# Kernel optimization log

Hardware: AMD Instinct MI355X
Metric: run time of the kernel (lower is better)

## Reference

```python
import jax, jax.numpy as jnp
import numpy as np

B, S, H, NH, MAXLEN = 4, 1024, 2048, 16, 1024
HD = H // NH  # head_dim = 128

def setup_inputs() -> dict:
    key = jax.random.key(0)
    ks = jax.random.split(key, 16)
    def lin(i):
        # torch Linear default init ~ U(-1/sqrt(in), 1/sqrt(in)); store W as [in, out]
        bound = 1.0 / np.sqrt(H)
        W = jax.random.uniform(ks[i], (H, H), jnp.float32, -bound, bound)
        b = jax.random.uniform(ks[i + 1], (H,), jnp.float32, -bound, bound)
        return W, b
    Wq, bq = lin(0)
    Wk, bk = lin(2)
    Wv, bv = lin(4)
    Wu, bu = lin(6)
    Wf2, bf2 = lin(8)
    rel_table = jax.random.normal(ks[10], (2 * MAXLEN - 1, NH), jnp.float32)
    query = jax.random.normal(ks[11], (B, S, H), jnp.float32)
    key_t = jax.random.normal(ks[12], (B, S, H), jnp.float32)
    value = jax.random.normal(ks[13], (B, S, H), jnp.float32)
    # causal mask [B, Sq, Sk]
    attn_mask = jnp.broadcast_to(jnp.tril(jnp.ones((S, S), bool)), (B, S, S))
    return {"query": query, "key": key_t, "value": value, "attn_mask": attn_mask,
            "Wq": Wq, "bq": bq, "Wk": Wk, "bk": bk, "Wv": Wv, "bv": bv,
            "Wu": Wu, "bu": bu, "Wf2": Wf2, "bf2": bf2, "rel_table": rel_table}

def reference(query, key, value, attn_mask, Wq, bq, Wk, bk, Wv, bv, Wu, bu, Wf2, bf2, rel_table):
    silu = jax.nn.silu
    U = silu(query @ Wu + bu)                      # [B,S,H]
    Q = silu(query @ Wq + bq).reshape(B, S, NH, HD).transpose(0, 2, 1, 3)  # [B,NH,S,HD]
    K = silu(key @ Wk + bk).reshape(B, S, NH, HD).transpose(0, 2, 1, 3)
    V = silu(value @ Wv + bv).reshape(B, S, NH, HD).transpose(0, 2, 1, 3)
    scale = HD ** -0.5
    scores = jnp.einsum('bhqd,bhkd->bhqk', Q, K) * scale  # [B,NH,S,S]
    # relative position bias lookup (non-infer path)
    positions = jnp.arange(S)[:, None] - jnp.arange(S)[None, :]
    rel_idx = positions + MAXLEN - 1                       # [S,S]
    rel_bias = rel_table[rel_idx].transpose(2, 0, 1)[None]  # [1,NH,S,S]
    scores = scores + rel_bias
    attn = silu(scores)  # SiLU attention instead of softmax
    attn = jnp.where(attn_mask[:, None, :, :], attn, 0.0)
    out = jnp.einsum('bhqk,bhkd->bhqd', attn, V)           # [B,NH,S,HD]
    out = out.transpose(0, 2, 1, 3).reshape(B, S, H)
    gated = out * U
    return gated @ Wf2 + bf2
```

## Files before the change

### kernel.cpp

```cpp
#include <hip/hip_runtime.h>
#include <stdint.h>

#define HDIM 2048
#define SEQLEN 1024
#define NHEADS 16
#define HEADD 128

typedef unsigned short u16;
typedef unsigned int u32;
typedef __attribute__((ext_vector_type(8))) short bf16x8;
typedef __attribute__((ext_vector_type(8))) u16 u16x8;
typedef __attribute__((ext_vector_type(4))) u16 u16x4;
typedef __attribute__((ext_vector_type(4))) float f32x4;

__device__ __forceinline__ float bf2f(u16 u) {
    union { u32 i; float f; } v; v.i = ((u32)u) << 16; return v.f;
}
__device__ __forceinline__ u16 f2bf(float f) {
    union { float f; u32 i; } v; v.f = f;
    return (u16)((v.i + 0x7fffu + ((v.i >> 16) & 1u)) >> 16);
}
__device__ __forceinline__ u16 f2bf_t(float f) {
    union { float f; u32 i; } v; v.f = f; return (u16)(v.i >> 16);
}
__device__ __forceinline__ float silu_f(float x) {
    return x * __builtin_amdgcn_rcpf(1.f + __expf(-x));
}
__device__ __forceinline__ void glds16(const void* g, void* l) {
    __builtin_amdgcn_global_load_lds(
        (const __attribute__((address_space(1))) u32*)g,
        (__attribute__((address_space(3))) u32*)l, 16, 0, 0);
}

__global__ __launch_bounds__(256) void f32_to_bf16(const float* __restrict__ in,
                                                   u16* __restrict__ out, int n8) {
    int i = blockIdx.x * 256 + threadIdx.x;
    const int stride = gridDim.x * 256;
    for (; i < n8; i += stride) {
        f32x4 a = *(const f32x4*)&in[(size_t)i * 8];
        f32x4 b = *(const f32x4*)&in[(size_t)i * 8 + 4];
        u16x8 o;
#pragma unroll
        for (int j = 0; j < 4; ++j) { o[j] = f2bf(a[j]); o[4 + j] = f2bf(b[j]); }
        *(u16x8*)&out[(size_t)i * 8] = o;
    }
}

__global__ __launch_bounds__(256) void transpose_w(const float* __restrict__ W,
                                                   u16* __restrict__ WT) {
    __shared__ u16 T[64][76];
    const int r0 = blockIdx.y * 64;
    const int c0 = blockIdx.x * 64;
    const int t = threadIdx.x;
#pragma unroll
    for (int c = t; c < 1024; c += 256) {
        const int r = c >> 4, cc = (c & 15) << 2;
        f32x4 v = *(const f32x4*)&W[(size_t)(r0 + r) * HDIM + c0 + cc];
        u16x4 o;
#pragma unroll
        for (int j = 0; j < 4; ++j) o[j] = f2bf(v[j]);
        *(u16x4*)&T[r][cc] = o;
    }
    __syncthreads();
#pragma unroll
    for (int c = t; c < 512; c += 256) {
        const int n = c >> 3, kc = (c & 7) << 3;
        u16x8 v;
#pragma unroll
        for (int j = 0; j < 8; ++j) v[j] = T[kc + j][n];
        *(u16x8*)&WT[(size_t)(c0 + n) * HDIM + r0 + kc] = v;
    }
}

__global__ __launch_bounds__(512, 2) void gemm256_8p(
    const u16* __restrict__ X,
    const u16* __restrict__ WTq, const u16* __restrict__ WTu,
    const float* __restrict__ bq, const float* __restrict__ bu,
    u16* __restrict__ Qo, u16* __restrict__ Uo)
{
    extern __shared__ u16 lds[];
    const int t = threadIdx.x;
    const int lane = t & 63, wid = t >> 6;
    const int l15 = lane & 15, l4 = lane >> 4;
    const int wr = wid >> 2, wn = wid & 3;

    const int bid = blockIdx.x;
    const int u = (bid & 7) * 32 + (bid >> 3);
    const int tm = u & 15, tn = u >> 4;
    const int m0 = tm * 256;
    const int n0 = tn * 256;
    const u16* WT = (n0 < 2048) ? WTq : WTu;
    const float* bias = (n0 < 2048) ? bq : bu;
    u16* outp = (n0 < 2048) ? Qo : Uo;
    const int nc0 = n0 & 2047;

    const int r64 = t >> 3;
    const int cse = (((t & 7) ^ (r64 & 7)) << 3);
    const u16* gA = X + (size_t)(m0 + r64) * HDIM + cse;
    const int rB0 = (r64 >> 5) * 64 + (r64 & 31);
    const u16* gB = WT + (size_t)(nc0 + rB0) * HDIM + cse;

    const int wbase = wid * 512;
    const int dstBw = (wid >> 2) * 4096 + (wid & 3) * 512;

    int offA[8][2], offB[4][2];
#pragma unroll
    for (int mf = 0; mf < 8; ++mf) {
        const int row = wr * 128 + mf * 16 + l15;
#pragma unroll
        for (int kk = 0; kk < 2; ++kk) {
            const int c = kk * 4 + l4;
            offA[mf][kk] = row * 64 + (((c) ^ (row & 7)) << 3);
        }
    }
#pragma unroll
    for (int nf = 0; nf < 4; ++nf) {
        const int row = wn * 64 + nf * 16 + l15;
#pragma unroll
        for (int kk = 0; kk < 2; ++kk) {
            const int c = kk * 4 + l4;
            offB[nf][kk] = 16384 + row * 64 + (((c) ^ (row & 7)) << 3);
        }
    }

#define SA(buf, rb, kt) glds16(gA + (size_t)(rb) * HDIM + (kt) * 64, \
                               lds + (buf) * 32768 + (rb) * 64 + wbase)
#define SB(buf, c, half, kt) glds16(gB + (size_t)((c) * 128 + (half) * 32) * HDIM + (kt) * 64, \
                               lds + (buf) * 32768 + 16384 + dstBw + (c) * 8192 + (half) * 2048)

    SA(0, 0, 0);    SA(0, 128, 0);
    SB(0, 0, 0, 0); SB(0, 1, 0, 0);
    SB(0, 0, 1, 0); SB(0, 1, 1, 0);
    SA(0, 64, 0);   SA(0, 192, 0);
    asm volatile("s_waitcnt vmcnt(2)" ::: "memory");
    __builtin_amdgcn_s_barrier();

    f32x4 acc[8][4] = {};
    int cur = 0;

#pragma unroll 1
    for (int kt = 0; kt < 32; ++kt) {
        const u16* pc = lds + cur * 32768;
        const int nb = cur ^ 1;
        const bool pf = (kt + 1 < 32);
        bf16x8 a[4][2], b[4][2];

#pragma unroll
        for (int mf = 0; mf < 4; ++mf)
#pragma unroll
            for (int kk = 0; kk < 2; ++kk)
                a[mf][kk] = *(const bf16x8*)(pc + offA[mf][kk]);
#pragma unroll
        for (int nf = 0; nf < 4; ++nf)
#pragma unroll
            for (int kk = 0; kk < 2; ++kk)
                b[nf][kk] = *(const bf16x8*)(pc + offB[nf][kk]);
        if (pf) { SA(nb, 0, kt + 1); SA(nb, 128, kt + 1);
                  SB(nb, 0, 0, kt + 1); SB(nb, 1, 0, kt + 1); }
        __builtin_amdgcn_s_setprio(1);
#pragma unroll
        for (int mf = 0; mf < 4; ++mf)
#pragma unroll
            for (int nf = 0; nf < 4; ++nf)
#pragma unroll
                for (int kk = 0; kk < 2; ++kk)
                    acc[mf][nf] = __builtin_amdgcn_mfma_f32_16x16x32_bf16(
                        a[mf][kk], b[nf][kk], acc[mf][nf], 0, 0, 0);
        __builtin_amdgcn_s_setprio(0);
        if (pf) { asm volatile("s_waitcnt vmcnt(4)" ::: "memory"); }
        else    { asm volatile("s_waitcnt vmcnt(0)" ::: "memory"); }
        __builtin_amdgcn_s_barrier();

#pragma unroll
        for (int mf = 0; mf < 4; ++mf)
#pragma unroll
            for (int kk = 0; kk < 2; ++kk)
                a[mf][kk] = *(const bf16x8*)(pc + offA[4 + mf][kk]);
        if (pf) { SB(nb, 0, 1, kt + 1); SB(nb, 1, 1, kt + 1);
                  SA(nb, 64, kt + 1);   SA(nb, 192, kt + 1); }
        __builtin_amdgcn_s_setprio(1);
#pragma unroll
        for (int mf = 0; mf < 4; ++mf)
#pragma unroll
            for (int nf = 0; nf < 4; ++nf)
#pragma unroll
                for (int kk = 0; kk < 2; ++kk)
                    acc[4 + mf][nf] = __builtin_amdgcn_mfma_f32_16x16x32_bf16(
                        a[mf][kk], b[nf][kk], acc[4 + mf][nf], 0, 0, 0);
        __builtin_amdgcn_s_setprio(0);
        if (pf) {
            asm volatile("s_waitcnt vmcnt(2)" ::: "memory");
            __builtin_amdgcn_s_barrier();
        }
        cur ^= 1;
    }
#undef SA
#undef SB

    float bvv[4];
#pragma unroll
    for (int nf = 0; nf < 4; ++nf) bvv[nf] = bias[nc0 + wn * 64 + nf * 16 + l15];
#pragma unroll
    for (int mf = 0; mf < 8; ++mf) {
        const int mbase = m0 + wr * 128 + mf * 16 + (l4 << 2);
#pragma unroll
        for (int r = 0; r < 4; ++r) {
            u16* rowp = outp + (size_t)(mbase + r) * HDIM + nc0 + wn * 64 + l15;
#pragma unroll
            for (int nf = 0; nf < 4; ++nf)
                rowp[nf * 16] = f2bf(silu_f(acc[mf][nf][r] + bvv[nf]));
        }
    }
}

__global__ __launch_bounds__(256) void gemm128(
    const u16* __restrict__ X, const u16* __restrict__ WT,
    const float* __restrict__ bias, void* __restrict__ outp, const int mode)
{
    extern __shared__ u16 lds[];
    const int t = threadIdx.x;
    const int lane = t & 63, wid = t >> 6;
    const int l15 = lane & 15, l4 = lane >> 4;
    const int wr = wid >> 1, wn = wid & 1;

    const int bid = blockIdx.x;
    const int u = (bid & 7) * 64 + (bid >> 3);
    const int tm = u & 31, tn = u >> 5;
    const int m0 = tm * 128, n0 = tn * 128;

    const int ric = t >> 3;
    const int cse = (((t & 7) ^ (ric & 7)) << 3);
    const u16* gA = X  + (size_t)(m0 + ric) * HDIM + cse;
    const u16* gB = WT + (size_t)(n0 + ric) * HDIM + cse;

    u16* buf0 = lds;
    u16* buf1 = lds + 16384;
    const int wbase = wid * 512;

    int offA[4][2], offB[4][2];
#pragma unroll
    for (int i = 0; i < 4; ++i) {
        const int row = wr * 64 + i * 16 + l15;
#pragma unroll
        for (int kk = 0; kk < 2; ++kk)
            offA[i][kk] = ((row * 128 + kk * 64 + l4 * 16) ^ ((row & 7) << 4)) >> 1;
    }
#pragma unroll
    for (int j = 0; j < 4; ++j) {
        const int row = wn * 64 + j * 16 + l15;
#pragma unroll
        for (int kk = 0; kk < 2; ++kk)
            offB[j][kk] = 8192 + ((((row * 128 + kk * 64 + l4 * 16) ^ ((row & 7) << 4))) >> 1);
    }

#define STAGE_A(buf, c, kt) glds16(gA + (size_t)(c) * 32 * HDIM + (kt) * 64, (buf) + (c) * 2048 + wbase)
#define STAGE_B(buf, c, kt) glds16(gB + (size_t)(c) * 32 * HDIM + (kt) * 64, (buf) + 8192 + (c) * 2048 + wbase)

    STAGE_B(buf0, 0, 0); STAGE_B(buf0, 1, 0); STAGE_B(buf0, 2, 0); STAGE_B(buf0, 3, 0);
    STAGE_A(buf0, 0, 0); STAGE_A(buf0, 1, 0); STAGE_A(buf0, 2, 0); STAGE_A(buf0, 3, 0);
    STAGE_B(buf1, 0, 1); STAGE_B(buf1, 1, 1); STAGE_B(buf1, 2, 1); STAGE_B(buf1, 3, 1);
    STAGE_A(buf1, 0, 1); STAGE_A(buf1, 2, 1);
    asm volatile("s_waitcnt vmcnt(6)" ::: "memory");
    __builtin_amdgcn_s_barrier();

    f32x4 acc[4][4] = {};
    u16* pc = buf0;
    u16* pn = buf1;

#pragma unroll 1
    for (int tt = 0; tt < 32; ++tt) {
        bf16x8 bfr[4][2], afr[2][2];
#pragma unroll
        for (int j = 0; j < 4; ++j)
#pragma unroll
            for (int kk = 0; kk < 2; ++kk)
                bfr[j][kk] = *(const bf16x8*)(pc + offB[j][kk]);
#pragma unroll
        for (int i = 0; i < 2; ++i)
#pragma unroll
            for (int kk = 0; kk < 2; ++kk)
                afr[i][kk] = *(const bf16x8*)(pc + offA[i][kk]);
        if (tt + 1 < 32) { STAGE_A(pn, 1, tt + 1); STAGE_A(pn, 3, tt + 1); }
        __builtin_amdgcn_s_setprio(1);
#pragma unroll
        for (int i = 0; i < 2; ++i)
#pragma unroll
            for (int j = 0; j < 4; ++j)
#pragma unroll
                for (int kk = 0; kk < 2; ++kk)
                    acc[i][j] = __builtin_amdgcn_mfma_f32_16x16x32_bf16(
                        afr[i][kk], bfr[j][kk], acc[i][j], 0, 0, 0);
        __builtin_amdgcn_s_setprio(0);
        __builtin_amdgcn_s_barrier();

#pragma unroll
        for (int i = 0; i < 2; ++i)
#pragma unroll
            for (int kk = 0; kk < 2; ++kk)
                afr[i][kk] = *(const bf16x8*)(pc + offA[2 + i][kk]);
        if (tt + 2 < 32) {
            STAGE_B(pc, 0, tt + 2); STAGE_B(pc, 1, tt + 2);
            STAGE_B(pc, 2, tt + 2); STAGE_B(pc, 3, tt + 2);
            STAGE_A(pc, 0, tt + 2); STAGE_A(pc, 2, tt + 2);
        }
        __builtin_amdgcn_s_setprio(1);
#pragma unroll
        for (int i = 0; i < 2; ++i)
#pragma unroll
            for (int j = 0; j < 4; ++j)
#pragma unroll
                for (int kk = 0; kk < 2; ++kk)
                    acc[2 + i][j] = __builtin_amdgcn_mfma_f32_16x16x32_bf16(
                        afr[i][kk], bfr[j][kk], acc[2 + i][j], 0, 0, 0);
        __builtin_amdgcn_s_setprio(0);
        if (tt + 2 < 32)      { asm volatile("s_waitcnt vmcnt(6)" ::: "memory"); }
        else if (tt + 1 < 32) { asm volatile("s_waitcnt vmcnt(0)" ::: "memory"); }
        __builtin_amdgcn_s_barrier();
        u16* tmp = pc; pc = pn; pn = tmp;
    }
#undef STAGE_A
#undef STAGE_B

    float bvv[4];
#pragma unroll
    for (int j = 0; j < 4; ++j) bvv[j] = bias[n0 + wn * 64 + j * 16 + l15];

    if (mode == 2) {
        u16* Tv = lds;
        __syncthreads();
#pragma unroll
        for (int i = 0; i < 4; ++i)
#pragma unroll
            for (int r = 0; r < 4; ++r) {
                const int s = wr * 64 + i * 16 + (l4 << 2) + r;
#pragma unroll
                for (int j = 0; j < 4; ++j) {
                    const int d = wn * 64 + j * 16 + l15;
                    Tv[d * 136 + s] = f2bf(silu_f(acc[i][j][r] + bvv[j]));
                }
            }
        __syncthreads();
        const int bh = (m0 >> 10) * 16 + tn;
        const int s0 = m0 & 1023;
        u16* vt = (u16*)outp;
#pragma unroll
        for (int r8 = 0; r8 < 8; ++r8) {
            const int d = (t >> 4) + r8 * 16;
            const int s = (t & 15) * 8;
            u16x8 v = *(const u16x8*)&Tv[d * 136 + s];
            *(u16x8*)&vt[((size_t)bh * HEADD + d) * SEQLEN + s0 + s] = v;
        }
        return;
    }

#pragma unroll
    for (int i = 0; i < 4; ++i) {
        const int mbase = m0 + wr * 64 + i * 16 + (l4 << 2);
#pragma unroll
        for (int r = 0; r < 4; ++r) {
            const size_t rowoff = (size_t)(mbase + r) * HDIM + n0 + wn * 64 + l15;
#pragma unroll
            for (int j = 0; j < 4; ++j) {
                const float v = acc[i][j][r] + bvv[j];
                if (mode == 0)
                    ((u16*)outp)[rowoff + j * 16] = f2bf(silu_f(v));
                else
                    ((float*)outp)[rowoff + j * 16] = v;
            }
        }
    }
}

__global__ __launch_bounds__(512) void attn_fused(
    const u16* __restrict__ Qb, const u16* __restrict__ Kb,
    const u16* __restrict__ VTg, const u16* __restrict__ Ub,
    const float* __restrict__ rel, u16* __restrict__ G)
{
    extern __shared__ u16 alds[];
    u16* Ps = alds + 24576;
    float* relh = (float*)(alds + 33792);

    const int idx = blockIdx.x;
    const int bh8 = idx & 7;
    const int j = (idx >> 3) & 7;
    const int bhhi = idx >> 6;
    const int bh = bhhi * 8 + bh8;
    const int b = bh >> 4, h = bh & 15;
    const int qS0 = j * 64;
    const int qL0 = (15 - j) * 64;
    const int nkt = 16 - j;
    const int t = threadIdx.x, lane = t & 63, w = t >> 6;
    const int wq = w & 3;
    const bool isL = (w < 4);
    const int l15 = lane & 15, l4 = lane >> 4, l3 = lane >> 3;
    const size_t rowbase = (size_t)b * SEQLEN;
    const int col0 = h * HEADD;
    const float scale = 0.088388347648318447f;

    for (int i = t; i < 1024; i += 512) relh[i] = rel[(size_t)(1023 + i) * NHEADS + h];

    const u16* gK0 = Kb + (rowbase + w * 8 + l4) * HDIM + col0 + ((lane & 15) ^ l4) * 8;
    const u16* gK1 = Kb + (rowbase + w * 8 + 4 + l4) * HDIM + col0 + ((lane & 15) ^ (l4 + 4)) * 8;
    const u16* gV0 = VTg + ((size_t)bh * HEADD + w * 16 + l3) * SEQLEN + ((lane & 7) ^ l3) * 8;
    const u16* gV1 = VTg + ((size_t)bh * HEADD + w * 16 + 8 + l3) * SEQLEN + ((lane & 7) ^ l3) * 8;

    const int q0 = (isL ? qL0 : qS0) + wq * 16;
    bf16x8 aq[4];
#pragma unroll
    for (int dc = 0; dc < 4; ++dc)
        aq[dc] = *(const bf16x8*)&Qb[(rowbase + q0 + l15) * HDIM + col0 + dc * 32 + (l4 << 3)];

    f32x4 oacc[8] = {};
    const int prB = (isL ? 0 : 64) + wq * 16;

#define STAGE_K(kt) do {                                                        \
    const size_t ko_ = (size_t)(kt) * 64 * HDIM;                                \
    glds16(gK0 + ko_, alds + w * 1024);                                         \
    glds16(gK1 + ko_, alds + w * 1024 + 512);                                   \
} while (0)
#define STAGE_V(kt, bsel) do {                                                  \
    u16* vb_ = alds + 8192 + ((bsel) ? 8192 : 0);                               \
    const size_t ko_ = (size_t)(kt) * 64;                                       \
    glds16(gV0 + ko_, vb_ + w * 1024);                                          \
    glds16(gV1 + ko_, vb_ + w * 1024 + 512);                                    \
} while (0)

    STAGE_K(0); STAGE_V(0, 0);
    asm volatile("s_waitcnt vmcnt(0)" ::: "memory");
    __builtin_amdgcn_s_barrier();

    int cur = 0;
#pragma unroll 1
    for (int kt = 0; kt < nkt; ++kt) {
        const int k0 = kt * 64;
        const bool act = isL || (kt <= j);
        const bool diag = isL ? (kt == nkt - 1) : (kt == j);
        if (kt + 1 < nkt) STAGE_V(kt + 1, cur ^ 1);
        const u16* kb = alds;
        const u16* vb = alds + 8192 + (cur ? 8192 : 0);

        if (act) {
#pragma unroll
            for (int kf = 0; kf < 4; ++kf) {
                const int krow = kf * 16 + l15;
                f32x4 s = {};
                __builtin_amdgcn_s_setprio(1);
#pragma unroll
                for (int dc = 0; dc < 4; ++dc) {
                    bf16x8 bk = *(const bf16x8*)&kb[krow * 128 + (((dc * 4 + l4) ^ (krow & 7)) << 3)];
                    s = __builtin_amdgcn_mfma_f32_16x16x32_bf16(aq[dc], bk, s, 0, 0, 0);
                }
                __builtin_amdgcn_s_setprio(0);
                const int kabs = k0 + krow;
                const int pr = prB + (l4 << 2);
                if (diag) {
#pragma unroll
                    for (int r = 0; r < 4; ++r) {
                        const int qabs = q0 + (l4 << 2) + r;
                        float v = 0.f;
                        if (kabs <= qabs) v = silu_f(fmaf(s[r], scale, relh[qabs - kabs]));
                        Ps[(pr + r) * 72 + kf * 16 + l15] = f2bf_t(v);
                    }
                } else {
#pragma unroll
                    for (int r = 0; r < 4; ++r) {
                        const int qabs = q0 + (l4 << 2) + r;
                        const float v = silu_f(fmaf(s[r], scale, relh[qabs - kabs]));
                        Ps[(pr + r) * 72 + kf * 16 + l15] = f2bf_t(v);
                    }
                }
            }
        }
        asm volatile("s_waitcnt lgkmcnt(0)" ::: "memory");
        __builtin_amdgcn_s_barrier();
        if (kt + 1 < nkt) STAGE_K(kt + 1);

        if (act) {
            bf16x8 ap[2];
#pragma unroll
            for (int kc = 0; kc < 2; ++kc)
                ap[kc] = *(const bf16x8*)&Ps[(prB + l15) * 72 + kc * 32 + (l4 << 3)];
            __builtin_amdgcn_s_setprio(1);
#pragma unroll
            for (int df = 0; df < 8; ++df) {
                const int vrow = df * 16 + l15;
#pragma unroll
                for (int kc = 0; kc < 2; ++kc) {
                    bf16x8 bv = *(const bf16x8*)&vb[vrow * 64 + (((kc * 4 + l4) ^ (vrow & 7)) << 3)];
                    oacc[df] = __builtin_amdgcn_mfma_f32_16x16x32_bf16(ap[kc], bv, oacc[df], 0, 0, 0);
                }
            }
            __builtin_amdgcn_s_setprio(0);
        }
        asm volatile("s_waitcnt vmcnt(0) lgkmcnt(0)" ::: "memory");
        __builtin_amdgcn_s_barrier();
        cur ^= 1;
    }
#undef STAGE_K
#undef STAGE_V

#pragma unroll
    for (int r = 0; r < 4; ++r) {
        const int qr = q0 + (l4 << 2) + r;
        const size_t row = (rowbase + qr) * HDIM + col0 + l15;
#pragma unroll
        for (int df = 0; df < 8; ++df)
            G[row + df * 16] = f2bf(oacc[df][r] * bf2f(Ub[row + df * 16]));
    }
}

extern "C" void kernel_launch(void* const* d_in, const int* in_sizes, int n_in,
                              void* d_out, int out_size, void* d_ws, size_t ws_size,
                              hipStream_t stream) {
    const float* query = (const float*)d_in[0];
    const float* key_  = (const float*)d_in[1];
    const float* value = (const float*)d_in[2];
    const float* Wq  = (const float*)d_in[4];  const float* bq  = (const float*)d_in[5];
    const float* Wk  = (const float*)d_in[6];  const float* bk  = (const float*)d_in[7];
    const float* Wv  = (const float*)d_in[8];  const float* bv  = (const float*)d_in[9];
    const float* Wu  = (const float*)d_in[10]; const float* bu  = (const float*)d_in[11];
    const float* Wf2 = (const float*)d_in[12]; const float* bf2 = (const float*)d_in[13];
    const float* rel = (const float*)d_in[14];

    char* ws = (char*)d_ws;
    const size_t WBYTES = (size_t)HDIM * HDIM * 2;
    const size_t ABYTES = (size_t)4096 * HDIM * 2;
    u16* WTa  = (u16*)ws;
    u16* Xbf  = (u16*)(ws + WBYTES);
    u16* Qbuf = (u16*)(ws + WBYTES + 1 * ABYTES);
    u16* Kbuf = (u16*)(ws + WBYTES + 2 * ABYTES);
    u16* VTg  = (u16*)(ws + WBYTES + 3 * ABYTES);
    u16* Ubuf = (u16*)(ws + WBYTES + 4 * ABYTES);
    u16* WTb  = VTg;
    u16* Gbuf = Qbuf;

    dim3 tpb(256);
    dim3 tgrid(32, 32);
    const int n8 = 4096 * HDIM / 8;
    const size_t GLDS  = 65536;
    const size_t G8LDS = 131072;
    const size_t ALDS  = 71680;

    f32_to_bf16<<<2048, tpb, 0, stream>>>(query, Xbf, n8);
    transpose_w<<<tgrid, tpb, 0, stream>>>(Wq, WTa);
    transpose_w<<<tgrid, tpb, 0, stream>>>(Wu, WTb);
    gemm256_8p<<<256, 512, G8LDS, stream>>>(Xbf, WTa, WTb, bq, bu, Qbuf, Ubuf);
    transpose_w<<<tgrid, tpb, 0, stream>>>(Wk, WTa);
    f32_to_bf16<<<2048, tpb, 0, stream>>>(key_, Xbf, n8);
    gemm128<<<512, tpb, GLDS, stream>>>(Xbf, WTa, bk, Kbuf, 0);
    transpose_w<<<tgrid, tpb, 0, stream>>>(Wv, WTa);
    f32_to_bf16<<<2048, tpb, 0, stream>>>(value, Xbf, n8);
    gemm128<<<512, tpb, GLDS, stream>>>(Xbf, WTa, bv, VTg, 2);
    attn_fused<<<512, 512, ALDS, stream>>>(Qbuf, Kbuf, VTg, Ubuf, rel, Gbuf);
    transpose_w<<<tgrid, tpb, 0, stream>>>(Wf2, WTa);
    gemm128<<<512, tpb, GLDS, stream>>>(Gbuf, WTa, bf2, d_out, 1);
}
```

Measured before the change: 293.1 us.

## Merge K and V projection GEMMs into one launch and simplify GEMM pipelining

Fuses the K and V projection GEMMs into a single 1024-block launch. The key activations and transposed Wv are staged in the output buffer as scratch so both inputs exist at once. Both GEMM kernels drop their split half-tile prefetch schedule: each iteration issues the whole next tile's loads up front, then waits with vmcnt(0) at the end. The attention kernel drops some lgkmcnt waits before barriers. Together these aim to fill the GPU with one larger launch and cut barrier count, at the cost of less overlap between loads and compute and a possible LDS race risk where the waits were removed.

New measurement: 290.6 us. About the same (-0.9%).

```diff
diff --git a/kernel.cpp b/kernel.cpp
--- a/kernel.cpp
+++ b/kernel.cpp
@@ -127,12 +127,13 @@
                                lds + (buf) * 32768 + (rb) * 64 + wbase)
 #define SB(buf, c, half, kt) glds16(gB + (size_t)((c) * 128 + (half) * 32) * HDIM + (kt) * 64, \
                                lds + (buf) * 32768 + 16384 + dstBw + (c) * 8192 + (half) * 2048)
-
-    SA(0, 0, 0);    SA(0, 128, 0);
-    SB(0, 0, 0, 0); SB(0, 1, 0, 0);
-    SB(0, 0, 1, 0); SB(0, 1, 1, 0);
-    SA(0, 64, 0);   SA(0, 192, 0);
-    asm volatile("s_waitcnt vmcnt(2)" ::: "memory");
+#define SALL(buf, kt) do {                                                     \
+    SA(buf, 0, kt); SA(buf, 64, kt); SA(buf, 128, kt); SA(buf, 192, kt);       \
+    SB(buf, 0, 0, kt); SB(buf, 1, 0, kt); SB(buf, 0, 1, kt); SB(buf, 1, 1, kt);\
+} while (0)
+
+    SALL(0, 0);
+    asm volatile("s_waitcnt vmcnt(0)" ::: "memory");
     __builtin_amdgcn_s_barrier();
 
     f32x4 acc[8][4] = {};
@@ -145,6 +146,7 @@
         const bool pf = (kt + 1 < 32);
         bf16x8 a[4][2], b[4][2];
 
+        if (pf) SALL(nb, kt + 1);
 #pragma unroll
         for (int mf = 0; mf < 4; ++mf)
 #pragma unroll
@@ -155,8 +157,6 @@
 #pragma unroll
             for (int kk = 0; kk < 2; ++kk)
                 b[nf][kk] = *(const bf16x8*)(pc + offB[nf][kk]);
-        if (pf) { SA(nb, 0, kt + 1); SA(nb, 128, kt + 1);
-                  SB(nb, 0, 0, kt + 1); SB(nb, 1, 0, kt + 1); }
         __builtin_amdgcn_s_setprio(1);
 #pragma unroll
         for (int mf = 0; mf < 4; ++mf)
@@ -167,17 +167,12 @@
                     acc[mf][nf] = __builtin_amdgcn_mfma_f32_16x16x32_bf16(
                         a[mf][kk], b[nf][kk], acc[mf][nf], 0, 0, 0);
         __builtin_amdgcn_s_setprio(0);
-        if (pf) { asm volatile("s_waitcnt vmcnt(4)" ::: "memory"); }
-        else    { asm volatile("s_waitcnt vmcnt(0)" ::: "memory"); }
-        __builtin_amdgcn_s_barrier();
 
 #pragma unroll
         for (int mf = 0; mf < 4; ++mf)
 #pragma unroll
             for (int kk = 0; kk < 2; ++kk)
                 a[mf][kk] = *(const bf16x8*)(pc + offA[4 + mf][kk]);
-        if (pf) { SB(nb, 0, 1, kt + 1); SB(nb, 1, 1, kt + 1);
-                  SA(nb, 64, kt + 1);   SA(nb, 192, kt + 1); }
         __builtin_amdgcn_s_setprio(1);
 #pragma unroll
         for (int mf = 0; mf < 4; ++mf)
@@ -188,12 +183,11 @@
                     acc[4 + mf][nf] = __builtin_amdgcn_mfma_f32_16x16x32_bf16(
                         a[mf][kk], b[nf][kk], acc[4 + mf][nf], 0, 0, 0);
         __builtin_amdgcn_s_setprio(0);
-        if (pf) {
-            asm volatile("s_waitcnt vmcnt(2)" ::: "memory");
-            __builtin_amdgcn_s_barrier();
-        }
+        if (pf) { asm volatile("s_waitcnt vmcnt(0)" ::: "memory"); }
+        __builtin_amdgcn_s_barrier();
         cur ^= 1;
     }
+#undef SALL
 #undef SA
 #undef SB
 
@@ -213,17 +207,16 @@
     }
 }
 
-__global__ __launch_bounds__(256) void gemm128(
+__device__ __forceinline__ void gemm128_body(
     const u16* __restrict__ X, const u16* __restrict__ WT,
-    const float* __restrict__ bias, void* __restrict__ outp, const int mode)
+    const float* __restrict__ bias, void* __restrict__ outp,
+    const int mode, const int bid, u16* lds)
 {
-    extern __shared__ u16 lds[];
     const int t = threadIdx.x;
     const int lane = t & 63, wid = t >> 6;
     const int l15 = lane & 15, l4 = lane >> 4;
     const int wr = wid >> 1, wn = wid & 1;
 
-    const int bid = blockIdx.x;
     const int u = (bid & 7) * 64 + (bid >> 3);
     const int tm = u & 31, tn = u >> 5;
     const int m0 = tm * 128, n0 = tn * 128;
@@ -253,14 +246,19 @@
             offB[j][kk] = 8192 + ((((row * 128 + kk * 64 + l4 * 16) ^ ((row & 7) << 4))) >> 1);
     }
 
-#define STAGE_A(buf, c, kt) glds16(gA + (size_t)(c) * 32 * HDIM + (kt) * 64, (buf) + (c) * 2048 + wbase)
-#define STAGE_B(buf, c, kt) glds16(gB + (size_t)(c) * 32 * HDIM + (kt) * 64, (buf) + 8192 + (c) * 2048 + wbase)
-
-    STAGE_B(buf0, 0, 0); STAGE_B(buf0, 1, 0); STAGE_B(buf0, 2, 0); STAGE_B(buf0, 3, 0);
-    STAGE_A(buf0, 0, 0); STAGE_A(buf0, 1, 0); STAGE_A(buf0, 2, 0); STAGE_A(buf0, 3, 0);
-    STAGE_B(buf1, 0, 1); STAGE_B(buf1, 1, 1); STAGE_B(buf1, 2, 1); STAGE_B(buf1, 3, 1);
-    STAGE_A(buf1, 0, 1); STAGE_A(buf1, 2, 1);
-    asm volatile("s_waitcnt vmcnt(6)" ::: "memory");
+#define STAGE_ALL(buf, kt) do {                                                 \
+    glds16(gB + (size_t)0 * 32 * HDIM + (kt) * 64, (buf) + 8192 + 0 * 2048 + wbase); \
+    glds16(gB + (size_t)1 * 32 * HDIM + (kt) * 64, (buf) + 8192 + 1 * 2048 + wbase); \
+    glds16(gB + (size_t)2 * 32 * HDIM + (kt) * 64, (buf) + 8192 + 2 * 2048 + wbase); \
+    glds16(gB + (size_t)3 * 32 * HDIM + (kt) * 64, (buf) + 8192 + 3 * 2048 + wbase); \
+    glds16(gA + (size_t)0 * 32 * HDIM + (kt) * 64, (buf) + 0 * 2048 + wbase);   \
+    glds16(gA + (size_t)1 * 32 * HDIM + (kt) * 64, (buf) + 1 * 2048 + wbase);   \
+    glds16(gA + (size_t)2 * 32 * HDIM + (kt) * 64, (buf) + 2 * 2048 + wbase);   \
+    glds16(gA + (size_t)3 * 32 * HDIM + (kt) * 64, (buf) + 3 * 2048 + wbase);   \
+} while (0)
+
+    STAGE_ALL(buf0, 0);
+    asm volatile("s_waitcnt vmcnt(0)" ::: "memory");
     __builtin_amdgcn_s_barrier();
 
     f32x4 acc[4][4] = {};
@@ -269,21 +267,21 @@
 
 #pragma unroll 1
     for (int tt = 0; tt < 32; ++tt) {
-        bf16x8 bfr[4][2], afr[2][2];
+        if (tt + 1 < 32) STAGE_ALL(pn, tt + 1);
+        bf16x8 bfr[4][2], afr[4][2];
 #pragma unroll
         for (int j = 0; j < 4; ++j)
 #pragma unroll
             for (int kk = 0; kk < 2; ++kk)
                 bfr[j][kk] = *(const bf16x8*)(pc + offB[j][kk]);
 #pragma unroll
-        for (int i = 0; i < 2; ++i)
+        for (int i = 0; i < 4; ++i)
 #pragma unroll
             for (int kk = 0; kk < 2; ++kk)
                 afr[i][kk] = *(const bf16x8*)(pc + offA[i][kk]);
-        if (tt + 1 < 32) { STAGE_A(pn, 1, tt + 1); STAGE_A(pn, 3, tt + 1); }
         __builtin_amdgcn_s_setprio(1);
 #pragma unroll
-        for (int i = 0; i < 2; ++i)
+        for (int i = 0; i < 4; ++i)
 #pragma unroll
             for (int j = 0; j < 4; ++j)
 #pragma unroll
@@ -291,35 +289,11 @@
                     acc[i][j] = __builtin_amdgcn_mfma_f32_16x16x32_bf16(
                         afr[i][kk], bfr[j][kk], acc[i][j], 0, 0, 0);
         __builtin_amdgcn_s_setprio(0);
-        __builtin_amdgcn_s_barrier();
-
-#pragma unroll
-        for (int i = 0; i < 2; ++i)
-#pragma unroll
-            for (int kk = 0; kk < 2; ++kk)
-                afr[i][kk] = *(const bf16x8*)(pc + offA[2 + i][kk]);
-        if (tt + 2 < 32) {
-            STAGE_B(pc, 0, tt + 2); STAGE_B(pc, 1, tt + 2);
-            STAGE_B(pc, 2, tt + 2); STAGE_B(pc, 3, tt + 2);
-            STAGE_A(pc, 0, tt + 2); STAGE_A(pc, 2, tt + 2);
-        }
-        __builtin_amdgcn_s_setprio(1);
-#pragma unroll
-        for (int i = 0; i < 2; ++i)
-#pragma unroll
-            for (int j = 0; j < 4; ++j)
-#pragma unroll
-                for (int kk = 0; kk < 2; ++kk)
-                    acc[2 + i][j] = __builtin_amdgcn_mfma_f32_16x16x32_bf16(
-                        afr[i][kk], bfr[j][kk], acc[2 + i][j], 0, 0, 0);
-        __builtin_amdgcn_s_setprio(0);
-        if (tt + 2 < 32)      { asm volatile("s_waitcnt vmcnt(6)" ::: "memory"); }
-        else if (tt + 1 < 32) { asm volatile("s_waitcnt vmcnt(0)" ::: "memory"); }
+        if (tt + 1 < 32) { asm volatile("s_waitcnt vmcnt(0)" ::: "memory"); }
         __builtin_amdgcn_s_barrier();
         u16* tmp = pc; pc = pn; pn = tmp;
     }
-#undef STAGE_A
-#undef STAGE_B
+#undef STAGE_ALL
 
     float bvv[4];
 #pragma unroll
@@ -369,6 +343,26 @@
             }
         }
     }
+}
+
+__global__ __launch_bounds__(256) void gemm128(
+    const u16* __restrict__ X, const u16* __restrict__ WT,
+    const float* __restrict__ bias, void* __restrict__ outp, const int mode)
+{
+    extern __shared__ u16 lds[];
+    gemm128_body(X, WT, bias, outp, mode, blockIdx.x, lds);
+}
+
+__global__ __launch_bounds__(256) void gemm128_kv(
+    const u16* __restrict__ Kx, const u16* __restrict__ WTk,
+    const float* __restrict__ bk, u16* __restrict__ Ko,
+    const u16* __restrict__ Vx, const u16* __restrict__ WTv,
+    const float* __restrict__ bv, u16* __restrict__ Vo)
+{
+    extern __shared__ u16 lds[];
+    const int bid = blockIdx.x;
+    if (bid < 512) gemm128_body(Kx, WTk, bk, Ko, 0, bid, lds);
+    else           gemm128_body(Vx, WTv, bv, Vo, 2, bid - 512, lds);
 }
 
 __global__ __launch_bounds__(512) void attn_fused(
@@ -471,7 +465,6 @@
                 }
             }
         }
-        asm volatile("s_waitcnt lgkmcnt(0)" ::: "memory");
         __builtin_amdgcn_s_barrier();
         if (kt + 1 < nkt) STAGE_K(kt + 1);
 
@@ -492,7 +485,7 @@
             }
             __builtin_amdgcn_s_setprio(0);
         }
-        asm volatile("s_waitcnt vmcnt(0) lgkmcnt(0)" ::: "memory");
+        asm volatile("s_waitcnt vmcnt(0)" ::: "memory");
         __builtin_amdgcn_s_barrier();
         cur ^= 1;
     }
@@ -533,6 +526,8 @@
     u16* Ubuf = (u16*)(ws + WBYTES + 4 * ABYTES);
     u16* WTb  = VTg;
     u16* Gbuf = Qbuf;
+    u16* KXbf = (u16*)d_out;
+    u16* WTv  = (u16*)((char*)d_out + ABYTES);
 
     dim3 tpb(256);
     dim3 tgrid(32, 32);
@@ -545,12 +540,12 @@
     transpose_w<<<tgrid, tpb, 0, stream>>>(Wq, WTa);
     transpose_w<<<tgrid, tpb, 0, stream>>>(Wu, WTb);
     gemm256_8p<<<256, 512, G8LDS, stream>>>(Xbf, WTa, WTb, bq, bu, Qbuf, Ubuf);
+    f32_to_bf16<<<2048, tpb, 0, stream>>>(key_, KXbf, n8);
+    f32_to_bf16<<<2048, tpb, 0, stream>>>(value, Xbf, n8);
     transpose_w<<<tgrid, tpb, 0, stream>>>(Wk, WTa);
-    f32_to_bf16<<<2048, tpb, 0, stream>>>(key_, Xbf, n8);
-    gemm128<<<512, tpb, GLDS, stream>>>(Xbf, WTa, bk, Kbuf, 0);
-    transpose_w<<<tgrid, tpb, 0, stream>>>(Wv, WTa);
-    f32_to_bf16<<<2048, tpb, 0, stream>>>(value, Xbf, n8);
-    gemm128<<<512, tpb, GLDS, stream>>>(Xbf, WTa, bv, VTg, 2);
+    transpose_w<<<tgrid, tpb, 0, stream>>>(Wv, WTv);
+    gemm128_kv<<<1024, tpb, GLDS, stream>>>(KXbf, WTa, bk, Kbuf,
+                                            Xbf, WTv, bv, VTg);
     attn_fused<<<512, 512, ALDS, stream>>>(Qbuf, Kbuf, VTg, Ubuf, rel, Gbuf);
     transpose_w<<<tgrid, tpb, 0, stream>>>(Wf2, WTa);
     gemm128<<<512, tpb, GLDS, stream>>>(Gbuf, WTa, bf2, d_out, 1);
```
